# Performance work log

Measured on AMD Instinct MI355X. Metric: run time of the kernel, lower is better.

The kernel has to match this reference:

```python
import jax, jax.numpy as jnp
import numpy as np

TEMPERATURE = 0.5
LAMBDA_REG = 0.1
NUM_GROUPS = 4  # number of distinct sensitive-attribute values
EPS = 1e-8      # torch cosine_similarity norm clamp


def setup_inputs() -> dict:
    key = jax.random.key(0)
    k1, k2, k3 = jax.random.split(key, 3)
    B, D = 4096, 256
    return {
        "z_i": jax.random.normal(k1, (B, D), dtype=jnp.float32),
        "z_j": jax.random.normal(k2, (B, D), dtype=jnp.float32),
        "sensitive_features": jax.random.randint(k3, (B,), 0, NUM_GROUPS, dtype=jnp.int64),
    }


def reference(z_i, z_j, sensitive_features):
    B = z_i.shape[0]
    z = jnp.concatenate([z_i, z_j], axis=0)                       # [2B, D]
    norm = jnp.maximum(jnp.linalg.norm(z, axis=1, keepdims=True), EPS)
    zn = z / norm                                                  # row-normalized
    S = zn @ zn.T                                                  # [2B, 2B] cosine sims

    # NT-Xent contrastive term
    pos = jnp.concatenate([jnp.diagonal(S, offset=B), jnp.diagonal(S, offset=-B)])  # [2B]
    mask = 1.0 - jnp.eye(2 * B, dtype=S.dtype)                     # zero out self-sims
    den = jnp.sum(mask * jnp.exp(S / TEMPERATURE), axis=1)         # [2B]
    contrastive = jnp.sum(-(pos / TEMPERATURE) + jnp.log(den)) / (2 * B)

    # Fairness penalty over groups of the FIRST B rows (indices come from sensitive_features)
    Sg = S[:B, :B]
    onehot = jax.nn.one_hot(sensitive_features, NUM_GROUPS, dtype=S.dtype)  # [B, G]
    group_sums = jnp.sum(onehot * (Sg @ onehot), axis=0)           # [G] sum_{i,j in g} S[i,j] (incl. diag, as torch)
    counts = jnp.sum(onehot, axis=0)                               # [G]
    per_group = jnp.where(counts > 1, group_sums / (counts * (counts - 1.0)), 0.0)
    num_unique = jnp.sum(counts > 0).astype(S.dtype)
    fairness = LAMBDA_REG * (jnp.sum(per_group) / num_unique)

    return contrastive + fairness
```

## Files before the change

kernel.cpp:

```cpp
#include <hip/hip_runtime.h>
#include <hip/hip_bf16.h>

typedef __attribute__((ext_vector_type(8))) short short8;
typedef __attribute__((ext_vector_type(4))) float f32x4;
typedef __attribute__((address_space(1))) const void gvoid_t;
typedef __attribute__((address_space(3))) void lvoid_t;

#define NB 4096
#define DD 256
#define TWOB 8192
#define NMACRO 2080u
#define GSUM_BLOCKS 16
#define NPART 2096u

__device__ __forceinline__ unsigned short f2bf(float f) {
  unsigned int u = __float_as_uint(f);
  u += 0x7fffu + ((u >> 16) & 1u);
  return (unsigned short)(u >> 16);
}
__device__ __forceinline__ float bf2f(unsigned short s) {
  return __uint_as_float(((unsigned int)s) << 16);
}


__global__ __launch_bounds__(256) void norm_kernel(const float* __restrict__ zi,
                                                   const float* __restrict__ zj,
                                                   float* __restrict__ wsf,
                                                   float* __restrict__ ppos,
                                                   unsigned short* __restrict__ znb) {
  __shared__ float sred[4];
  if (blockIdx.x < 32) wsf[blockIdx.x * 256 + threadIdx.x] = 0.f;
  const int lane = threadIdx.x & 63, wave = threadIdx.x >> 6;
  const int i = blockIdx.x * 4 + wave;

  float4 a = ((const float4*)(zi + (size_t)i * DD))[lane];
  float4 b = ((const float4*)(zj + (size_t)i * DD))[lane];
  float sa = a.x * a.x + a.y * a.y + a.z * a.z + a.w * a.w;
  float sb = b.x * b.x + b.y * b.y + b.z * b.z + b.w * b.w;
  float sab = a.x * b.x + a.y * b.y + a.z * b.z + a.w * b.w;
#pragma unroll
  for (int m = 32; m >= 1; m >>= 1) {
    sa += __shfl_xor(sa, m);
    sb += __shfl_xor(sb, m);
    sab += __shfl_xor(sab, m);
  }
  float ra = 1.0f / fmaxf(sqrtf(sa), 1e-8f);
  float rb = 1.0f / fmaxf(sqrtf(sb), 1e-8f);
  ushort4 oa, ob;
  oa.x = f2bf(a.x * ra); oa.y = f2bf(a.y * ra); oa.z = f2bf(a.z * ra); oa.w = f2bf(a.w * ra);
  ob.x = f2bf(b.x * rb); ob.y = f2bf(b.y * rb); ob.z = f2bf(b.z * rb); ob.w = f2bf(b.w * rb);
  ((ushort4*)(znb + (size_t)i * DD))[lane] = oa;
  ((ushort4*)(znb + (size_t)(i + NB) * DD))[lane] = ob;

  if (lane == 0) sred[wave] = sab * ra * rb;
  __syncthreads();
  if (threadIdx.x == 0)
    ppos[blockIdx.x] = sred[0] + sred[1] + sred[2] + sred[3];
}

__global__ __launch_bounds__(256, 3) void den_kernel(const int* __restrict__ sf,
                                                     float* __restrict__ wsf,
                                                     const unsigned short* __restrict__ znb,
                                                     float* __restrict__ vsum_part,
                                                     int* __restrict__ cnt_part) {
  __shared__ __align__(16) unsigned short As[3][4096];
  __shared__ __align__(16) unsigned short Bs[3][4096];

  float* den = wsf;

  const int tid = threadIdx.x;
  const int lane = tid & 63, wave = tid >> 6;
  const unsigned t_raw = blockIdx.y * 64u + blockIdx.x;
  if (t_raw >= NPART) return;
  const unsigned t_lin = (t_raw & 7u) * 262u + (t_raw >> 3);

  if (t_lin < GSUM_BLOCKS) {
    const int b = (int)t_lin;
    const int r0 = b * 256;
    float acc[4][4];
#pragma unroll
    for (int q = 0; q < 4; ++q)
#pragma unroll
      for (int e = 0; e < 4; ++e) acc[q][e] = 0.f;
    int cnt[4] = {0, 0, 0, 0};
    const int rw = r0 + wave * 64;
    for (int k = 0; k < 64; ++k) {
      int row = rw + k;
      int g = sf[row];
      ushort4 v = ((const ushort4*)(znb + (size_t)row * DD))[lane];
      float f0 = bf2f(v.x), f1 = bf2f(v.y), f2 = bf2f(v.z), f3 = bf2f(v.w);
#pragma unroll
      for (int q = 0; q < 4; ++q) {
        bool sel = (g == q);
        acc[q][0] += sel ? f0 : 0.f;
        acc[q][1] += sel ? f1 : 0.f;
        acc[q][2] += sel ? f2 : 0.f;
        acc[q][3] += sel ? f3 : 0.f;
        cnt[q] += sel ? 1 : 0;
      }
    }
    float4* lsd = (float4*)&As[0][0];
    int* lcnt = (int*)&Bs[0][0];
#pragma unroll
    for (int q = 0; q < 4; ++q) {
      float4 t;
      t.x = acc[q][0]; t.y = acc[q][1]; t.z = acc[q][2]; t.w = acc[q][3];
      lsd[(wave * 4 + q) * 64 + lane] = t;
    }
    if (lane == 0) {
#pragma unroll
      for (int q = 0; q < 4; ++q) lcnt[wave * 4 + q] = cnt[q];
    }
    __syncthreads();
    {
      int g = tid >> 6, l = tid & 63;
      float4 s0 = lsd[(0 + g) * 64 + l];
      float4 s1 = lsd[(4 + g) * 64 + l];
      float4 s2 = lsd[(8 + g) * 64 + l];
      float4 s3 = lsd[(12 + g) * 64 + l];
      float4 s;
      s.x = s0.x + s1.x + s2.x + s3.x;
      s.y = s0.y + s1.y + s2.y + s3.y;
      s.z = s0.z + s1.z + s2.z + s3.z;
      s.w = s0.w + s1.w + s2.w + s3.w;
      ((float4*)(vsum_part + (size_t)(b * 4 + g) * 256))[l] = s;
      if (tid < 4)
        cnt_part[b * 4 + tid] = lcnt[tid] + lcnt[4 + tid] + lcnt[8 + tid] + lcnt[12 + tid];
    }
    return;
  }

  unsigned t = t_lin - GSUM_BLOCKS;
  unsigned i = 0;
  while (t >= 64u - i) { t -= 64u - i; ++i; }
  unsigned j = i + t;
  const size_t rowbase = (size_t)i * 128;
  const size_t colbase = (size_t)j * 128;
  const bool offdiag = (j > i);

  const int u = lane >> 3;
  const int cp = (lane & 7) ^ u;
  const int ri = 2 * u + (cp >> 2);
  const int kelem = (cp & 3) * 8;
  const int slot = ((((lane & 1) << 2) | (lane >> 4)) ^ ((lane >> 1) & 7));
  const int fragoff = ((lane & 15) >> 1) * 128 + slot * 16;
  const int wrow = wave & 1;
  const int wcol = wave >> 1;

  f32x4 zero = {0.f, 0.f, 0.f, 0.f};
  f32x4 acc[4][4];
#pragma unroll
  for (int a = 0; a < 4; ++a)
#pragma unroll
    for (int b2 = 0; b2 < 4; ++b2) acc[a][b2] = zero;

  const unsigned short* gA0 = znb + (rowbase + (2 * wave) * 16 + ri) * DD + kelem;
  const unsigned short* gA1 = gA0 + 16 * DD;
  const unsigned short* gB0 = znb + (colbase + (2 * wave) * 16 + ri) * DD + kelem;
  const unsigned short* gB1 = gB0 + 16 * DD;

  auto stage = [&](int kt, int buf) {
    __builtin_amdgcn_global_load_lds((gvoid_t*)(gA0 + kt * 32), (lvoid_t*)&As[buf][(2 * wave) * 512], 16, 0, 0);
    __builtin_amdgcn_global_load_lds((gvoid_t*)(gA1 + kt * 32), (lvoid_t*)&As[buf][(2 * wave + 1) * 512], 16, 0, 0);
    __builtin_amdgcn_global_load_lds((gvoid_t*)(gB0 + kt * 32), (lvoid_t*)&Bs[buf][(2 * wave) * 512], 16, 0, 0);
    __builtin_amdgcn_global_load_lds((gvoid_t*)(gB1 + kt * 32), (lvoid_t*)&Bs[buf][(2 * wave + 1) * 512], 16, 0, 0);
  };

  stage(0, 0);
  stage(1, 1);
#pragma unroll
  for (int kt = 0; kt < 8; ++kt) {
    const int buf = kt % 3;
    if (kt < 7) asm volatile("s_waitcnt vmcnt(4)" ::: "memory");
    else        asm volatile("s_waitcnt vmcnt(0)" ::: "memory");
    __builtin_amdgcn_s_barrier();
    asm volatile("" ::: "memory");
    if (kt < 6) stage(kt + 2, (kt + 2) % 3);
    short8 af[4], bfr[4];
#pragma unroll
    for (int mi = 0; mi < 4; ++mi)
      af[mi] = *(const short8*)((const char*)&As[0][0] + buf * 8192 + (wrow * 4 + mi) * 1024 + fragoff);
#pragma unroll
    for (int ni = 0; ni < 4; ++ni)
      bfr[ni] = *(const short8*)((const char*)&Bs[0][0] + buf * 8192 + (wcol * 4 + ni) * 1024 + fragoff);
#pragma unroll
    for (int mi = 0; mi < 4; ++mi)
#pragma unroll
      for (int ni = 0; ni < 4; ++ni)
        acc[mi][ni] = __builtin_amdgcn_mfma_f32_16x16x32_bf16(af[mi], bfr[ni], acc[mi][ni], 0, 0, 0);
  }

  float rsum[4][4];
  float csum[4];
#pragma unroll
  for (int mi = 0; mi < 4; ++mi)
#pragma unroll
    for (int r = 0; r < 4; ++r) rsum[mi][r] = 0.f;
#pragma unroll
  for (int ni = 0; ni < 4; ++ni) csum[ni] = 0.f;
#pragma unroll
  for (int mi = 0; mi < 4; ++mi)
#pragma unroll
    for (int ni = 0; ni < 4; ++ni)
#pragma unroll
      for (int r = 0; r < 4; ++r) {
        float e = __expf(2.0f * acc[mi][ni][r]);
        rsum[mi][r] += e;
        csum[ni] += e;
      }
#pragma unroll
  for (int m = 1; m < 16; m <<= 1)
#pragma unroll
    for (int mi = 0; mi < 4; ++mi)
#pragma unroll
      for (int r = 0; r < 4; ++r) rsum[mi][r] += __shfl_xor(rsum[mi][r], m);
#pragma unroll
  for (int m = 16; m < 64; m <<= 1)
#pragma unroll
    for (int ni = 0; ni < 4; ++ni) csum[ni] += __shfl_xor(csum[ni], m);

  float* Lr = (float*)&As[0][0];
  float* Lc = Lr + 256;
  if ((lane & 15) == 0) {
    int h = lane >> 4;
#pragma unroll
    for (int mi = 0; mi < 4; ++mi)
#pragma unroll
      for (int r = 0; r < 4; ++r)
        Lr[wcol * 128 + wrow * 64 + mi * 16 + h * 4 + r] = rsum[mi][r];
  }
  if (lane < 16) {
#pragma unroll
    for (int ni = 0; ni < 4; ++ni)
      Lc[wrow * 128 + wcol * 64 + ni * 16 + lane] = csum[ni];
  }
  __syncthreads();
  if (tid < 128) {
    unsafeAtomicAdd(&den[rowbase + tid], Lr[tid] + Lr[128 + tid]);
  } else if (offdiag) {
    int cc = tid - 128;
    unsafeAtomicAdd(&den[colbase + cc], Lc[cc] + Lc[128 + cc]);
  }
}

__global__ __launch_bounds__(1024) void tail_kernel(const float* __restrict__ wsf,
                                                    const float* __restrict__ vsum_part,
                                                    const int* __restrict__ cnt_part,
                                                    const float* __restrict__ ppos,
                                                    float* __restrict__ out) {
  __shared__ float sred[48];
  const float* den = wsf;
  const int tid = threadIdx.x;
  const int lane = tid & 63, wave = tid >> 6;

  const float e2 = __expf(2.0f);
  float ls = 0.f;
#pragma unroll
  for (int k = 0; k < 8; ++k) ls += __logf(den[k * 1024 + tid] - e2);
#pragma unroll
  for (int m = 32; m >= 1; m >>= 1) ls += __shfl_xor(ls, m);
  if (lane == 0) sred[wave] = ls;

  float pp = ppos[tid];
#pragma unroll
  for (int m = 32; m >= 1; m >>= 1) pp += __shfl_xor(pp, m);
  if (lane == 0) sred[16 + wave] = pp;

  {
    int g = tid >> 8, col = tid & 255;
    float v = 0.f;
#pragma unroll
    for (int b = 0; b < 16; ++b) v += vsum_part[(size_t)(b * 4 + g) * 256 + col];
    float gp = v * v;
#pragma unroll
    for (int m = 32; m >= 1; m >>= 1) gp += __shfl_xor(gp, m);
    if (lane == 0) sred[32 + wave] = gp;
  }
  __syncthreads();
  if (tid == 0) {
    float lsum = 0.f, psum = 0.f;
#pragma unroll
    for (int w = 0; w < 16; ++w) { lsum += sred[w]; psum += sred[16 + w]; }
    float contrastive = (lsum - 4.0f * psum) / (float)TWOB;
    float fsum = 0.f;
    int uniq = 0;
#pragma unroll
    for (int q = 0; q < 4; ++q) {
      int ci = 0;
#pragma unroll
      for (int b = 0; b < 16; ++b) ci += cnt_part[b * 4 + q];
      float gsq = sred[32 + q * 4] + sred[33 + q * 4] + sred[34 + q * 4] + sred[35 + q * 4];
      float cf = (float)ci;
      if (ci > 0) uniq++;
      if (ci > 1) fsum += gsq / (cf * (cf - 1.0f));
    }
    out[0] = contrastive + 0.1f * (fsum / (uniq > 0 ? (float)uniq : 1.0f));
  }
}

extern "C" void kernel_launch(void* const* d_in, const int* in_sizes, int n_in,
                              void* d_out, int out_size, void* d_ws, size_t ws_size,
                              hipStream_t stream) {
  const float* zi = (const float*)d_in[0];
  const float* zj = (const float*)d_in[1];
  const int* sf = (const int*)d_in[2];
  float* out = (float*)d_out;
  char* ws = (char*)d_ws;
  float* wsf = (float*)ws;
  unsigned short* znb = (unsigned short*)(ws + 65536);
  float* vsum_part = (float*)(ws + 4259840);
  int* cnt_part = (int*)(ws + 4276224);
  float* ppos = (float*)(ws + 4276480);

  hipLaunchKernelGGL(norm_kernel, dim3(1024), dim3(256), 0, stream, zi, zj, wsf, ppos, znb);
  hipLaunchKernelGGL(den_kernel, dim3(64, 33), dim3(256), 0, stream,
                     sf, wsf, znb, vsum_part, cnt_part);
  hipLaunchKernelGGL(tail_kernel, dim3(1), dim3(1024), 0, stream,
                     wsf, vsum_part, cnt_part, ppos, out);
}
```

Measured before the change: 98.51 us.

## Load MFMA fragments directly from global into registers, dropping LDS staging

Replaces the triple-buffered global_load_lds staging and its barriers with per-wave direct global loads of bf16 fragments into registers, software-pipelined one K-step ahead. LDS use shrinks to a small scratch buffer and launch bounds drop to 2 waves per EU. This removes the block barriers and LDS round trip, but each wave now fetches its own A/B rows, so the 2x2 wave grid loads every row twice instead of sharing it. Global loads are 16-byte reads strided by row and rely on L1/L2 for reuse.

Result: slower. 140.8 us (+43.0%).

```diff
diff --git a/kernel.cpp b/kernel.cpp
--- a/kernel.cpp
+++ b/kernel.cpp
@@ -3,8 +3,6 @@
 
 typedef __attribute__((ext_vector_type(8))) short short8;
 typedef __attribute__((ext_vector_type(4))) float f32x4;
-typedef __attribute__((address_space(1))) const void gvoid_t;
-typedef __attribute__((address_space(3))) void lvoid_t;
 
 #define NB 4096
 #define DD 256
@@ -58,13 +56,12 @@
     ppos[blockIdx.x] = sred[0] + sred[1] + sred[2] + sred[3];
 }
 
-__global__ __launch_bounds__(256, 3) void den_kernel(const int* __restrict__ sf,
+__global__ __launch_bounds__(256, 2) void den_kernel(const int* __restrict__ sf,
                                                      float* __restrict__ wsf,
                                                      const unsigned short* __restrict__ znb,
                                                      float* __restrict__ vsum_part,
                                                      int* __restrict__ cnt_part) {
-  __shared__ __align__(16) unsigned short As[3][4096];
-  __shared__ __align__(16) unsigned short Bs[3][4096];
+  __shared__ __align__(16) float Scr[4112];
 
   float* den = wsf;
 
@@ -99,8 +96,8 @@
         cnt[q] += sel ? 1 : 0;
       }
     }
-    float4* lsd = (float4*)&As[0][0];
-    int* lcnt = (int*)&Bs[0][0];
+    float4* lsd = (float4*)&Scr[0];
+    int* lcnt = (int*)&Scr[4096];
 #pragma unroll
     for (int q = 0; q < 4; ++q) {
       float4 t;
@@ -138,14 +135,19 @@
   const size_t colbase = (size_t)j * 128;
   const bool offdiag = (j > i);
 
-  const int u = lane >> 3;
-  const int cp = (lane & 7) ^ u;
-  const int ri = 2 * u + (cp >> 2);
-  const int kelem = (cp & 3) * 8;
-  const int slot = ((((lane & 1) << 2) | (lane >> 4)) ^ ((lane >> 1) & 7));
-  const int fragoff = ((lane & 15) >> 1) * 128 + slot * 16;
   const int wrow = wave & 1;
   const int wcol = wave >> 1;
+  const int frow = lane & 15;
+  const int fk = (lane >> 4) * 8;
+
+  const unsigned short* pA[4];
+  const unsigned short* pB[4];
+#pragma unroll
+  for (int mi = 0; mi < 4; ++mi)
+    pA[mi] = znb + (size_t)(rowbase + wrow * 64 + mi * 16 + frow) * DD + fk;
+#pragma unroll
+  for (int ni = 0; ni < 4; ++ni)
+    pB[ni] = znb + (size_t)(colbase + wcol * 64 + ni * 16 + frow) * DD + fk;
 
   f32x4 zero = {0.f, 0.f, 0.f, 0.f};
   f32x4 acc[4][4];
@@ -154,40 +156,30 @@
 #pragma unroll
     for (int b2 = 0; b2 < 4; ++b2) acc[a][b2] = zero;
 
-  const unsigned short* gA0 = znb + (rowbase + (2 * wave) * 16 + ri) * DD + kelem;
-  const unsigned short* gA1 = gA0 + 16 * DD;
-  const unsigned short* gB0 = znb + (colbase + (2 * wave) * 16 + ri) * DD + kelem;
-  const unsigned short* gB1 = gB0 + 16 * DD;
-
-  auto stage = [&](int kt, int buf) {
-    __builtin_amdgcn_global_load_lds((gvoid_t*)(gA0 + kt * 32), (lvoid_t*)&As[buf][(2 * wave) * 512], 16, 0, 0);
-    __builtin_amdgcn_global_load_lds((gvoid_t*)(gA1 + kt * 32), (lvoid_t*)&As[buf][(2 * wave + 1) * 512], 16, 0, 0);
-    __builtin_amdgcn_global_load_lds((gvoid_t*)(gB0 + kt * 32), (lvoid_t*)&Bs[buf][(2 * wave) * 512], 16, 0, 0);
-    __builtin_amdgcn_global_load_lds((gvoid_t*)(gB1 + kt * 32), (lvoid_t*)&Bs[buf][(2 * wave + 1) * 512], 16, 0, 0);
-  };
-
-  stage(0, 0);
-  stage(1, 1);
+  short8 cA[4], cB[4], nA[4], nB[4];
+#pragma unroll
+  for (int mi = 0; mi < 4; ++mi) cA[mi] = *(const short8*)(pA[mi]);
+#pragma unroll
+  for (int ni = 0; ni < 4; ++ni) cB[ni] = *(const short8*)(pB[ni]);
 #pragma unroll
   for (int kt = 0; kt < 8; ++kt) {
-    const int buf = kt % 3;
-    if (kt < 7) asm volatile("s_waitcnt vmcnt(4)" ::: "memory");
-    else        asm volatile("s_waitcnt vmcnt(0)" ::: "memory");
-    __builtin_amdgcn_s_barrier();
-    asm volatile("" ::: "memory");
-    if (kt < 6) stage(kt + 2, (kt + 2) % 3);
-    short8 af[4], bfr[4];
+    if (kt < 7) {
+#pragma unroll
+      for (int mi = 0; mi < 4; ++mi) nA[mi] = *(const short8*)(pA[mi] + (kt + 1) * 32);
+#pragma unroll
+      for (int ni = 0; ni < 4; ++ni) nB[ni] = *(const short8*)(pB[ni] + (kt + 1) * 32);
+    }
 #pragma unroll
     for (int mi = 0; mi < 4; ++mi)
-      af[mi] = *(const short8*)((const char*)&As[0][0] + buf * 8192 + (wrow * 4 + mi) * 1024 + fragoff);
-#pragma unroll
-    for (int ni = 0; ni < 4; ++ni)
-      bfr[ni] = *(const short8*)((const char*)&Bs[0][0] + buf * 8192 + (wcol * 4 + ni) * 1024 + fragoff);
-#pragma unroll
-    for (int mi = 0; mi < 4; ++mi)
 #pragma unroll
       for (int ni = 0; ni < 4; ++ni)
-        acc[mi][ni] = __builtin_amdgcn_mfma_f32_16x16x32_bf16(af[mi], bfr[ni], acc[mi][ni], 0, 0, 0);
+        acc[mi][ni] = __builtin_amdgcn_mfma_f32_16x16x32_bf16(cA[mi], cB[ni], acc[mi][ni], 0, 0, 0);
+    if (kt < 7) {
+#pragma unroll
+      for (int mi = 0; mi < 4; ++mi) cA[mi] = nA[mi];
+#pragma unroll
+      for (int ni = 0; ni < 4; ++ni) cB[ni] = nB[ni];
+    }
   }
 
   float rsum[4][4];
@@ -219,8 +211,8 @@
 #pragma unroll
     for (int ni = 0; ni < 4; ++ni) csum[ni] += __shfl_xor(csum[ni], m);
 
-  float* Lr = (float*)&As[0][0];
-  float* Lc = Lr + 256;
+  float* Lr = &Scr[0];
+  float* Lc = &Scr[256];
   if ((lane & 15) == 0) {
     int h = lane >> 4;
 #pragma unroll
```
